# Kernel tuning notes

Hardware: AMD Instinct MI355X
Metric: run time of the kernel (lower is better)

Reference implementation:

```python
import jax, jax.numpy as jnp
import numpy as np

B, T, C, H = 2, 2048, 2048, 16
D = C // H  # head size = 128
ROPE_BASE = 10000.0


def setup_inputs() -> dict:
    key = jax.random.key(0)
    k1, k2, k3 = jax.random.split(key, 3)
    scale = 1.0 / np.sqrt(C)
    x = jax.random.normal(k1, (B, T, C), dtype=jnp.float32)
    w_qkv = jax.random.normal(k2, (3 * C, C), dtype=jnp.float32) * scale
    w_o = jax.random.normal(k3, (C, C), dtype=jnp.float32) * scale
    # rope cache: complex exp(i * pos * theta_j), stored as cos/sin, shape [T, D//2]
    inv_freq = 1.0 / (ROPE_BASE ** (np.arange(0, D, 2, dtype=np.float32) / D))  # [D//2]
    angles = np.arange(T, dtype=np.float32)[:, None] * inv_freq[None, :]        # [T, D//2]
    rope_cos = jnp.asarray(np.cos(angles))
    rope_sin = jnp.asarray(np.sin(angles))
    return {"x": x, "w_qkv": w_qkv, "w_o": w_o, "rope_cos": rope_cos, "rope_sin": rope_sin}


def _apply_rope(x, cos, sin):
    # x: [B, T, H, D]; cos/sin: [T, D//2]
    xr = x.reshape(*x.shape[:-1], D // 2, 2)
    x0, x1 = xr[..., 0], xr[..., 1]
    c = cos[None, :, None, :]
    s = sin[None, :, None, :]
    # complex multiply (x0 + i x1) * (c + i s)
    out = jnp.stack([x0 * c - x1 * s, x0 * s + x1 * c], axis=-1)
    return out.reshape(x.shape)


def reference(x, w_qkv, w_o, rope_cos, rope_sin):
    Bs, Ts, Cs = x.shape
    qkv = jnp.einsum('btc,ec->bte', x, w_qkv)  # [B, T, 3C]
    q, k, v = jnp.split(qkv, 3, axis=-1)
    q = q.reshape(Bs, Ts, H, D)
    k = k.reshape(Bs, Ts, H, D)
    v = v.reshape(Bs, Ts, H, D)
    q = _apply_rope(q, rope_cos[:Ts], rope_sin[:Ts])
    k = _apply_rope(k, rope_cos[:Ts], rope_sin[:Ts])
    scores = jnp.einsum('bthd,bshd->bhts', q, k) / jnp.sqrt(jnp.float32(D))
    causal = jnp.tril(jnp.ones((Ts, Ts), dtype=bool))
    scores = jnp.where(causal[None, None], scores, jnp.finfo(scores.dtype).min)
    attn = jax.nn.softmax(scores, axis=-1)
    y = jnp.einsum('bhts,bshd->bthd', attn, v).reshape(Bs, Ts, Cs)
    return jnp.einsum('btc,oc->bto', y, w_o)
```

## Files before the change

### kernel.cpp

```cpp
#include <hip/hip_runtime.h>
#include <cstdint>
#include <cstddef>

#define DEVI __device__ __forceinline__

typedef __attribute__((ext_vector_type(8))) short short8;
typedef __attribute__((ext_vector_type(4))) float f32x4;
typedef __attribute__((ext_vector_type(16))) float f32x16;
typedef __attribute__((ext_vector_type(4))) unsigned int u32x4;

static constexpr int Bdim = 2, T = 2048, C = 2048, H = 16, D = 128;
static constexpr int CQ = 3 * C;

DEVI unsigned short f2bf(float f) {
  unsigned int u = __float_as_uint(f);
  u = (u + 0x7fffu + ((u >> 16) & 1u)) >> 16;
  return (unsigned short)u;
}
DEVI float bf2f(unsigned int u) { return __uint_as_float(u << 16); }

DEVI unsigned int cvtpk(float lo, float hi) {
  unsigned int r;
  asm("v_cvt_pk_bf16_f32 %0, %1, %2" : "=v"(r) : "v"(lo), "v"(hi));
  return r;
}

DEVI void gload_lds16(const void* g, void* l) {
  __builtin_amdgcn_global_load_lds((const __attribute__((address_space(1))) void*)g,
                                   (__attribute__((address_space(3))) void*)l, 16, 0, 0);
}

__global__ __launch_bounds__(256) void convert_all(const float* __restrict__ x,
                                                   const float* __restrict__ wqkv,
                                                   const float* __restrict__ wo,
                                                   unsigned short* __restrict__ xb,
                                                   unsigned short* __restrict__ wqkvb,
                                                   unsigned short* __restrict__ wob) {
  int bid = blockIdx.x;
  const float* src;
  unsigned short* dst;
  if (bid < 8192) {
    src = x; dst = xb;
  } else if (bid < 8192 + 12288) {
    bid -= 8192; src = wqkv; dst = wqkvb;
  } else {
    bid -= 8192 + 12288; src = wo; dst = wob;
  }
  const int i = (bid * 256 + threadIdx.x) * 4;
  float4 v = *(const float4*)&src[i];
  uint2 o;
  o.x = (unsigned)f2bf(v.x) | ((unsigned)f2bf(v.y) << 16);
  o.y = (unsigned)f2bf(v.z) | ((unsigned)f2bf(v.w) << 16);
  *(uint2*)&dst[i] = o;
}

template <int OUT_BF16>
__global__ __launch_bounds__(256) void gemm_bt(const unsigned short* __restrict__ A,
                                               const unsigned short* __restrict__ Bm,
                                               void* __restrict__ outp,
                                               int M, int N, int Kd) {
  __shared__ __align__(16) unsigned short lds_a[128 * 64];
  __shared__ __align__(16) unsigned short lds_b[128 * 64];
  const int tid = threadIdx.x;
  const int wid = tid >> 6, lane = tid & 63;
  const int lg = lane >> 4, lc = lane & 15;
  const int m0 = blockIdx.y * 128, n0 = blockIdx.x * 128;
  const int wr = (wid >> 1) * 64, wc = (wid & 1) * 64;
  const int srow = wid * 8 + (lane >> 3);
  const int schunk = lane & 7;

  f32x4 acc[4][4] = {};

  for (int k0 = 0; k0 < Kd; k0 += 64) {
    __syncthreads();
#pragma unroll
    for (int j = 0; j < 4; ++j) {
      const int row = j * 32 + srow;
      const int cc = schunk ^ (row & 7);
      gload_lds16(&A[(size_t)(m0 + row) * Kd + k0 + cc * 8], &lds_a[j * 2048 + wid * 512]);
      gload_lds16(&Bm[(size_t)(n0 + row) * Kd + k0 + cc * 8], &lds_b[j * 2048 + wid * 512]);
    }
    __syncthreads();
    __builtin_amdgcn_s_setprio(1);
#pragma unroll
    for (int kk = 0; kk < 2; ++kk) {
      short8 af[4], bf[4];
#pragma unroll
      for (int m = 0; m < 4; ++m) {
        const int row = wr + m * 16 + lc;
        af[m] = *(const short8*)&lds_a[row * 64 + (((kk * 4 + lg) ^ (row & 7)) * 8)];
      }
#pragma unroll
      for (int n = 0; n < 4; ++n) {
        const int row = wc + n * 16 + lc;
        bf[n] = *(const short8*)&lds_b[row * 64 + (((kk * 4 + lg) ^ (row & 7)) * 8)];
      }
#pragma unroll
      for (int m = 0; m < 4; ++m)
#pragma unroll
        for (int n = 0; n < 4; ++n)
          acc[m][n] = __builtin_amdgcn_mfma_f32_16x16x32_bf16(af[m], bf[n], acc[m][n], 0, 0, 0);
    }
    __builtin_amdgcn_s_setprio(0);
  }

#pragma unroll
  for (int m = 0; m < 4; ++m)
#pragma unroll
    for (int n = 0; n < 4; ++n)
#pragma unroll
      for (int r = 0; r < 4; ++r) {
        const int row = m0 + wr + m * 16 + lg * 4 + r;
        const int col = n0 + wc + n * 16 + lc;
        const float v = acc[m][n][r];
        if (OUT_BF16)
          ((unsigned short*)outp)[(size_t)row * N + col] = f2bf(v);
        else
          ((float*)outp)[(size_t)row * N + col] = v;
      }
}

__global__ __launch_bounds__(256) void rope_vt_kernel(const unsigned short* __restrict__ qkv,
                                                      const float* __restrict__ cosb,
                                                      const float* __restrict__ sinb,
                                                      unsigned short* __restrict__ Qr,
                                                      unsigned short* __restrict__ Kr,
                                                      unsigned short* __restrict__ Vt) {
  if (blockIdx.x < 16384) {
    const int idx = blockIdx.x * 256 + threadIdx.x;
    const int i = idx & 63;
    const int h = (idx >> 6) & (H - 1);
    const int tg = idx >> 10;
    const int t = tg & (T - 1);
    const int b = tg >> 11;
    const float c = cosb[t * 64 + i], s = sinb[t * 64 + i];
    const unsigned short* row = qkv + (size_t)tg * CQ;
    const unsigned int q = *(const unsigned int*)&row[h * D + 2 * i];
    const unsigned int k = *(const unsigned int*)&row[C + h * D + 2 * i];
    const float q0 = bf2f(q & 0xffffu), q1 = bf2f(q >> 16);
    const float k0 = bf2f(k & 0xffffu), k1 = bf2f(k >> 16);
    const float SC = 0.08838834764831845f * 1.4426950408889634f;
    const float q0r = (q0 * c - q1 * s) * SC, q1r = (q0 * s + q1 * c) * SC;
    const float k0r = k0 * c - k1 * s, k1r = k0 * s + k1 * c;
    const size_t off = ((size_t)(b * H + h) * T + t) * D + 2 * i;
    *(unsigned int*)&Qr[off] = (unsigned)f2bf(q0r) | ((unsigned)f2bf(q1r) << 16);
    *(unsigned int*)&Kr[off] = (unsigned)f2bf(k0r) | ((unsigned)f2bf(k1r) << 16);
  } else {
    __shared__ unsigned short tile[64][65];
    const int bid2 = blockIdx.x - 16384;
    const int t0 = (bid2 & 31) * 64;
    const int d0 = ((bid2 >> 5) & 1) * 64;
    const int bh = bid2 >> 6, b = bh >> 4, h = bh & (H - 1);
    const int tx = threadIdx.x & 63, ty = threadIdx.x >> 6;
#pragma unroll
    for (int rr = 0; rr < 64; rr += 4)
      tile[rr + ty][tx] = qkv[(size_t)(b * T + t0 + rr + ty) * CQ + 2 * C + h * D + d0 + tx];
    __syncthreads();
#pragma unroll
    for (int rr = 0; rr < 64; rr += 4)
      Vt[((size_t)bh * D + d0 + rr + ty) * T + t0 + tx] = tile[tx][rr + ty];
  }
}

__global__ __launch_bounds__(256, 2) void flash_attn(const unsigned short* __restrict__ Q,
                                                     const unsigned short* __restrict__ K,
                                                     const unsigned short* __restrict__ Vt,
                                                     unsigned short* __restrict__ Y) {
  __shared__ __align__(16) unsigned short ldsK[64 * 128];
  __shared__ __align__(16) unsigned short ldsV[64 * 128];

  const int bid = blockIdx.x;
  const int lid = (bid & 7) * 64 + (bid >> 3);
  const int bh = lid >> 4;
  const int qt = 15 - (lid & 15);
  const int wid = threadIdx.x >> 6;
  const int lane = threadIdx.x & 63;
  const int l31 = lane & 31, l15 = lane & 15;
  const int hi = lane >> 5;
  const int b = bh >> 4, h = bh & (H - 1);
  const int q0w = qt * 128 + wid * 32;
  const int qrow = q0w + l31;

  const unsigned short* Qh = Q + (size_t)bh * T * D;
  const unsigned short* Kh = K + (size_t)bh * T * D;
  const unsigned short* Vh = Vt + (size_t)bh * D * T;

  const int sr = lane >> 4;

  short8 qf[8];
#pragma unroll
  for (int ds = 0; ds < 8; ++ds)
    qf[ds] = *(const short8*)&Qh[(size_t)qrow * D + ds * 16 + hi * 8];

  f32x16 oacc[4] = {};
  float m_run = -1e30f, l_run = 0.f;

  u32x4 rK[4], rV[4];

#pragma unroll
  for (int j = 0; j < 4; ++j) {
    const int r0 = (wid * 4 + j) * 4;
    const int row = r0 + sr;
    const int cc = l15 ^ (row & 15);
    rK[j] = *(const u32x4*)&Kh[(size_t)row * D + cc * 8];
    const int cv = l15 ^ (row & 15);
    const int d = row + ((cv >> 3) << 6);
    rV[j] = *(const u32x4*)&Vh[(size_t)d * T + (cv & 7) * 8];
  }

  const int ntb = 2 * qt + 2;
  for (int t = 0; t < ntb; ++t) {
    const int kv0 = t * 64;

    __builtin_amdgcn_s_barrier();

#pragma unroll
    for (int j = 0; j < 4; ++j) {
      const int r0 = (wid * 4 + j) * 4;
      *(u32x4*)((char*)ldsK + r0 * 256 + lane * 16) = rK[j];
      *(u32x4*)((char*)ldsV + r0 * 256 + lane * 16) = rV[j];
    }
    asm volatile("s_waitcnt lgkmcnt(0)" ::: "memory");
    __builtin_amdgcn_s_barrier();
    __builtin_amdgcn_sched_barrier(0);

    if (t + 1 < ntb) {
      const int kvn = kv0 + 64;
#pragma unroll
      for (int j = 0; j < 4; ++j) {
        const int r0 = (wid * 4 + j) * 4;
        const int row = r0 + sr;
        const int cc = l15 ^ (row & 15);
        rK[j] = *(const u32x4*)&Kh[(size_t)(kvn + row) * D + cc * 8];
        const int d = row + ((cc >> 3) << 6);
        rV[j] = *(const u32x4*)&Vh[(size_t)d * T + kvn + (cc & 7) * 8];
      }
    }
    __builtin_amdgcn_sched_barrier(0);

    if (kv0 <= q0w + 31) {
      f32x16 s0 = {}, s1 = {};
      __builtin_amdgcn_s_setprio(1);
#pragma unroll
      for (int ds = 0; ds < 8; ++ds) {
        const int cs = ((ds * 2 + hi) ^ l15) * 8;
        const short8 k0 = *(const short8*)&ldsK[l31 * 128 + cs];
        const short8 k1 = *(const short8*)&ldsK[(32 + l31) * 128 + cs];
        s0 = __builtin_amdgcn_mfma_f32_32x32x16_bf16(k0, qf[ds], s0, 0, 0, 0);
        s1 = __builtin_amdgcn_mfma_f32_32x32x16_bf16(k1, qf[ds], s1, 0, 0, 0);
      }
      __builtin_amdgcn_s_setprio(0);

      if (kv0 + 63 > q0w) {
#pragma unroll
        for (int r = 0; r < 16; ++r) {
          const int kvr = kv0 + (r & 3) + 8 * (r >> 2) + 4 * hi;
          s0[r] = (kvr <= qrow) ? s0[r] : -1e30f;
          s1[r] = (kvr + 32 <= qrow) ? s1[r] : -1e30f;
        }
      }

      float mt[8];
#pragma unroll
      for (int r = 0; r < 8; ++r)
        mt[r] = fmaxf(fmaxf(s0[r], s0[r + 8]), fmaxf(s1[r], s1[r + 8]));
#pragma unroll
      for (int r = 0; r < 4; ++r) mt[r] = fmaxf(mt[r], mt[r + 4]);
      float mx = fmaxf(fmaxf(mt[0], mt[1]), fmaxf(mt[2], mt[3]));
      mx = fmaxf(mx, __shfl_xor(mx, 32));
      const float mnew = fmaxf(m_run, mx);
      if (__any(mnew > m_run)) {
        const float f = exp2f(m_run - mnew);
        m_run = mnew;
        l_run *= f;
#pragma unroll
        for (int blk = 0; blk < 4; ++blk) oacc[blk] *= f;
      }
#pragma unroll
      for (int r = 0; r < 16; ++r) {
        s0[r] = exp2f(s0[r] - m_run);
        s1[r] = exp2f(s1[r] - m_run);
      }
      {
        float a0 = 0.f, a1 = 0.f, a2 = 0.f, a3 = 0.f;
#pragma unroll
        for (int r = 0; r < 16; r += 4) {
          a0 += s0[r] + s1[r];
          a1 += s0[r + 1] + s1[r + 1];
          a2 += s0[r + 2] + s1[r + 2];
          a3 += s0[r + 3] + s1[r + 3];
        }
        l_run += (a0 + a1) + (a2 + a3);
      }

      __builtin_amdgcn_s_setprio(1);
#pragma unroll
      for (int ks = 0; ks < 4; ++ks) {
        const int rb = (ks & 1) * 8;
        const f32x16& S = (ks < 2) ? s0 : s1;
        const unsigned int w0 = cvtpk(S[rb + 0], S[rb + 1]);
        const unsigned int w1 = cvtpk(S[rb + 2], S[rb + 3]);
        const unsigned int w2 = cvtpk(S[rb + 4], S[rb + 5]);
        const unsigned int w3 = cvtpk(S[rb + 6], S[rb + 7]);
        const unsigned int x0 = (unsigned int)__shfl_xor((int)w0, 32);
        const unsigned int x1 = (unsigned int)__shfl_xor((int)w1, 32);
        const unsigned int x2 = (unsigned int)__shfl_xor((int)w2, 32);
        const unsigned int x3 = (unsigned int)__shfl_xor((int)w3, 32);
        u32x4 av;
        av[0] = hi ? x2 : w0;
        av[1] = hi ? x3 : w1;
        av[2] = hi ? w2 : x0;
        av[3] = hi ? w3 : x1;
        const short8 pf = __builtin_bit_cast(short8, av);
#pragma unroll
        for (int blk = 0; blk < 4; ++blk) {
          const int row2 = (blk & 1) * 32 + l31;
          const int cs = ((((blk >> 1) * 8) + ks * 2 + hi) ^ l15) * 8;
          const short8 vf = *(const short8*)&ldsV[row2 * 128 + cs];
          oacc[blk] = __builtin_amdgcn_mfma_f32_32x32x16_bf16(vf, pf, oacc[blk], 0, 0, 0);
        }
      }
      __builtin_amdgcn_s_setprio(0);
    }
  }

  const float l = l_run + __shfl_xor(l_run, 32);
  const float inv = 1.0f / l;
  unsigned short* yrow = Y + ((size_t)(b * T + qrow)) * C + h * D;
#pragma unroll
  for (int blk = 0; blk < 4; ++blk)
#pragma unroll
    for (int g = 0; g < 4; ++g) {
      const int d0 = blk * 32 + 8 * g + 4 * hi;
      uint2 st;
      st.x = cvtpk(oacc[blk][4 * g + 0] * inv, oacc[blk][4 * g + 1] * inv);
      st.y = cvtpk(oacc[blk][4 * g + 2] * inv, oacc[blk][4 * g + 3] * inv);
      *(uint2*)&yrow[d0] = st;
    }
}

extern "C" void kernel_launch(void* const* d_in, const int* in_sizes, int n_in,
                              void* d_out, int out_size, void* d_ws, size_t ws_size,
                              hipStream_t stream) {
  const float* x = (const float*)d_in[0];
  const float* wqkv = (const float*)d_in[1];
  const float* wo = (const float*)d_in[2];
  const float* rc = (const float*)d_in[3];
  const float* rs = (const float*)d_in[4];
  float* out = (float*)d_out;
  char* ws = (char*)d_ws;

  unsigned short* xb    = (unsigned short*)(ws + 0);
  unsigned short* wqkvb = (unsigned short*)(ws + 16777216);
  unsigned short* qkv   = (unsigned short*)(ws + 41943040);
  unsigned short* Qr    = (unsigned short*)(ws + 92274688);
  unsigned short* Kr    = (unsigned short*)(ws + 109051904);
  unsigned short* wob   = (unsigned short*)(ws + 125829120);
  unsigned short* Vt  = xb;
  unsigned short* Yb  = qkv;

  convert_all<<<8192 + 12288 + 4096, 256, 0, stream>>>(x, wqkv, wo, xb, wqkvb, wob);
  gemm_bt<1><<<dim3(CQ / 128, (Bdim * T) / 128), 256, 0, stream>>>(xb, wqkvb, (void*)qkv,
                                                                   Bdim * T, CQ, C);
  rope_vt_kernel<<<18432, 256, 0, stream>>>(qkv, rc, rs, Qr, Kr, Vt);
  flash_attn<<<512, 256, 0, stream>>>(Qr, Kr, Vt, Yb);
  gemm_bt<0><<<dim3(C / 128, (Bdim * T) / 128), 256, 0, stream>>>(Yb, wob, (void*)out,
                                                                  Bdim * T, C, C);
}
```

Baseline: 267.2 us.

## Fuse RoPE into flash attention and keep only V transpose pre-pass

Removes the separate RoPE kernel that wrote rotated Q and K buffers. The attention kernel now reads Q and K directly from the qkv projection output and applies the rotation in registers while loading, with the K rotation done before the LDS store. A standalone V transpose kernel remains. This saves a full write and read of Q/K, but it adds cos/sin loads and rotation ALU work for every K tile visit, which raises register pressure and redundant compute.

New measurement: 306.1 us. 1.15x slower.

```diff
diff --git a/kernel.cpp b/kernel.cpp
--- a/kernel.cpp
+++ b/kernel.cpp
@@ -120,51 +120,25 @@
       }
 }
 
-__global__ __launch_bounds__(256) void rope_vt_kernel(const unsigned short* __restrict__ qkv,
-                                                      const float* __restrict__ cosb,
-                                                      const float* __restrict__ sinb,
-                                                      unsigned short* __restrict__ Qr,
-                                                      unsigned short* __restrict__ Kr,
-                                                      unsigned short* __restrict__ Vt) {
-  if (blockIdx.x < 16384) {
-    const int idx = blockIdx.x * 256 + threadIdx.x;
-    const int i = idx & 63;
-    const int h = (idx >> 6) & (H - 1);
-    const int tg = idx >> 10;
-    const int t = tg & (T - 1);
-    const int b = tg >> 11;
-    const float c = cosb[t * 64 + i], s = sinb[t * 64 + i];
-    const unsigned short* row = qkv + (size_t)tg * CQ;
-    const unsigned int q = *(const unsigned int*)&row[h * D + 2 * i];
-    const unsigned int k = *(const unsigned int*)&row[C + h * D + 2 * i];
-    const float q0 = bf2f(q & 0xffffu), q1 = bf2f(q >> 16);
-    const float k0 = bf2f(k & 0xffffu), k1 = bf2f(k >> 16);
-    const float SC = 0.08838834764831845f * 1.4426950408889634f;
-    const float q0r = (q0 * c - q1 * s) * SC, q1r = (q0 * s + q1 * c) * SC;
-    const float k0r = k0 * c - k1 * s, k1r = k0 * s + k1 * c;
-    const size_t off = ((size_t)(b * H + h) * T + t) * D + 2 * i;
-    *(unsigned int*)&Qr[off] = (unsigned)f2bf(q0r) | ((unsigned)f2bf(q1r) << 16);
-    *(unsigned int*)&Kr[off] = (unsigned)f2bf(k0r) | ((unsigned)f2bf(k1r) << 16);
-  } else {
-    __shared__ unsigned short tile[64][65];
-    const int bid2 = blockIdx.x - 16384;
-    const int t0 = (bid2 & 31) * 64;
-    const int d0 = ((bid2 >> 5) & 1) * 64;
-    const int bh = bid2 >> 6, b = bh >> 4, h = bh & (H - 1);
-    const int tx = threadIdx.x & 63, ty = threadIdx.x >> 6;
-#pragma unroll
-    for (int rr = 0; rr < 64; rr += 4)
-      tile[rr + ty][tx] = qkv[(size_t)(b * T + t0 + rr + ty) * CQ + 2 * C + h * D + d0 + tx];
-    __syncthreads();
-#pragma unroll
-    for (int rr = 0; rr < 64; rr += 4)
-      Vt[((size_t)bh * D + d0 + rr + ty) * T + t0 + tx] = tile[tx][rr + ty];
-  }
-}
-
-__global__ __launch_bounds__(256, 2) void flash_attn(const unsigned short* __restrict__ Q,
-                                                     const unsigned short* __restrict__ K,
+__global__ __launch_bounds__(256) void transpose_v(const unsigned short* __restrict__ qkv,
+                                                   unsigned short* __restrict__ Vt) {
+  __shared__ unsigned short tile[64][65];
+  const int bh = blockIdx.z, b = bh >> 4, h = bh & (H - 1);
+  const int t0 = blockIdx.x * 64, d0 = blockIdx.y * 64;
+  const int tx = threadIdx.x & 63, ty = threadIdx.x >> 6;
+#pragma unroll
+  for (int rr = 0; rr < 64; rr += 4)
+    tile[rr + ty][tx] = qkv[(size_t)(b * T + t0 + rr + ty) * CQ + 2 * C + h * D + d0 + tx];
+  __syncthreads();
+#pragma unroll
+  for (int rr = 0; rr < 64; rr += 4)
+    Vt[((size_t)bh * D + d0 + rr + ty) * T + t0 + tx] = tile[tx][rr + ty];
+}
+
+__global__ __launch_bounds__(256, 2) void flash_attn(const unsigned short* __restrict__ qkv,
                                                      const unsigned short* __restrict__ Vt,
+                                                     const float* __restrict__ cosb,
+                                                     const float* __restrict__ sinb,
                                                      unsigned short* __restrict__ Y) {
   __shared__ __align__(16) unsigned short ldsK[64 * 128];
   __shared__ __align__(16) unsigned short ldsV[64 * 128];
@@ -181,31 +155,45 @@
   const int q0w = qt * 128 + wid * 32;
   const int qrow = q0w + l31;
 
-  const unsigned short* Qh = Q + (size_t)bh * T * D;
-  const unsigned short* Kh = K + (size_t)bh * T * D;
+  const unsigned short* Qq = qkv + (size_t)(b * T) * CQ + h * D;
+  const unsigned short* Kq = qkv + (size_t)(b * T) * CQ + C + h * D;
   const unsigned short* Vh = Vt + (size_t)bh * D * T;
 
   const int sr = lane >> 4;
 
+  const float SC = 0.08838834764831845f * 1.4426950408889634f;
   short8 qf[8];
 #pragma unroll
-  for (int ds = 0; ds < 8; ++ds)
-    qf[ds] = *(const short8*)&Qh[(size_t)qrow * D + ds * 16 + hi * 8];
+  for (int ds = 0; ds < 8; ++ds) {
+    const int d0 = ds * 16 + hi * 8;
+    const u32x4 raw = *(const u32x4*)&Qq[(size_t)qrow * CQ + d0];
+    const f32x4 c4 = *(const f32x4*)&cosb[qrow * 64 + (d0 >> 1)];
+    const f32x4 s4 = *(const f32x4*)&sinb[qrow * 64 + (d0 >> 1)];
+    u32x4 w;
+#pragma unroll
+    for (int e = 0; e < 4; ++e) {
+      const float x0 = bf2f(raw[e] & 0xffffu), x1 = bf2f(raw[e] >> 16);
+      w[e] = cvtpk((x0 * c4[e] - x1 * s4[e]) * SC, (x0 * s4[e] + x1 * c4[e]) * SC);
+    }
+    qf[ds] = __builtin_bit_cast(short8, w);
+  }
 
   f32x16 oacc[4] = {};
   float m_run = -1e30f, l_run = 0.f;
 
   u32x4 rK[4], rV[4];
+  f32x4 rC[4], rS[4];
 
 #pragma unroll
   for (int j = 0; j < 4; ++j) {
     const int r0 = (wid * 4 + j) * 4;
     const int row = r0 + sr;
     const int cc = l15 ^ (row & 15);
-    rK[j] = *(const u32x4*)&Kh[(size_t)row * D + cc * 8];
-    const int cv = l15 ^ (row & 15);
-    const int d = row + ((cv >> 3) << 6);
-    rV[j] = *(const u32x4*)&Vh[(size_t)d * T + (cv & 7) * 8];
+    rK[j] = *(const u32x4*)&Kq[(size_t)row * CQ + cc * 8];
+    rC[j] = *(const f32x4*)&cosb[row * 64 + cc * 4];
+    rS[j] = *(const f32x4*)&sinb[row * 64 + cc * 4];
+    const int d = row + ((cc >> 3) << 6);
+    rV[j] = *(const u32x4*)&Vh[(size_t)d * T + (cc & 7) * 8];
   }
 
   const int ntb = 2 * qt + 2;
@@ -217,7 +205,13 @@
 #pragma unroll
     for (int j = 0; j < 4; ++j) {
       const int r0 = (wid * 4 + j) * 4;
-      *(u32x4*)((char*)ldsK + r0 * 256 + lane * 16) = rK[j];
+      u32x4 w;
+#pragma unroll
+      for (int e = 0; e < 4; ++e) {
+        const float x0 = bf2f(rK[j][e] & 0xffffu), x1 = bf2f(rK[j][e] >> 16);
+        w[e] = cvtpk(x0 * rC[j][e] - x1 * rS[j][e], x0 * rS[j][e] + x1 * rC[j][e]);
+      }
+      *(u32x4*)((char*)ldsK + r0 * 256 + lane * 16) = w;
       *(u32x4*)((char*)ldsV + r0 * 256 + lane * 16) = rV[j];
     }
     asm volatile("s_waitcnt lgkmcnt(0)" ::: "memory");
@@ -231,7 +225,9 @@
         const int r0 = (wid * 4 + j) * 4;
         const int row = r0 + sr;
         const int cc = l15 ^ (row & 15);
-        rK[j] = *(const u32x4*)&Kh[(size_t)(kvn + row) * D + cc * 8];
+        rK[j] = *(const u32x4*)&Kq[(size_t)(kvn + row) * CQ + cc * 8];
+        rC[j] = *(const f32x4*)&cosb[(kvn + row) * 64 + cc * 4];
+        rS[j] = *(const f32x4*)&sinb[(kvn + row) * 64 + cc * 4];
         const int d = row + ((cc >> 3) << 6);
         rV[j] = *(const u32x4*)&Vh[(size_t)d * T + kvn + (cc & 7) * 8];
       }
@@ -353,17 +349,15 @@
   unsigned short* xb    = (unsigned short*)(ws + 0);
   unsigned short* wqkvb = (unsigned short*)(ws + 16777216);
   unsigned short* qkv   = (unsigned short*)(ws + 41943040);
-  unsigned short* Qr    = (unsigned short*)(ws + 92274688);
-  unsigned short* Kr    = (unsigned short*)(ws + 109051904);
+  unsigned short* Yb    = (unsigned short*)(ws + 92274688);
+  unsigned short* Vt    = (unsigned short*)(ws + 109051904);
   unsigned short* wob   = (unsigned short*)(ws + 125829120);
-  unsigned short* Vt  = xb;
-  unsigned short* Yb  = qkv;
 
   convert_all<<<8192 + 12288 + 4096, 256, 0, stream>>>(x, wqkv, wo, xb, wqkvb, wob);
   gemm_bt<1><<<dim3(CQ / 128, (Bdim * T) / 128), 256, 0, stream>>>(xb, wqkvb, (void*)qkv,
                                                                    Bdim * T, CQ, C);
-  rope_vt_kernel<<<18432, 256, 0, stream>>>(qkv, rc, rs, Qr, Kr, Vt);
-  flash_attn<<<512, 256, 0, stream>>>(Qr, Kr, Vt, Yb);
+  transpose_v<<<dim3(T / 64, D / 64, Bdim * H), 256, 0, stream>>>(qkv, Vt);
+  flash_attn<<<512, 256, 0, stream>>>(qkv, Vt, rc, rs, Yb);
   gemm_bt<0><<<dim3(C / 128, (Bdim * T) / 128), 256, 0, stream>>>(Yb, wob, (void*)out,
                                                                   Bdim * T, C, C);
 }
```

## Split causal attention KV range into two halves and merge with a combine kernel

Applied to the files above, without the earlier changes.

Each query tile's causal KV loop is split into two halves, run by separate blocks, so the flash-attention grid doubles from 512 to 1024 blocks. The aim is to cut the critical path of the longest causal tiles and improve load balance across CUs. Each half writes a bf16 partial output plus per-row (max, sum) statistics. A new combine kernel rescales and merges the two partials before the output projection. The cost is an extra launch, extra global traffic for two partial outputs and the stats, and an extra bf16 rounding of the partials.

Result: no change. 262.0 us (median of 3 runs) (-1.9%).

```diff
diff --git a/kernel.cpp b/kernel.cpp
--- a/kernel.cpp
+++ b/kernel.cpp
@@ -165,14 +165,17 @@
 __global__ __launch_bounds__(256, 2) void flash_attn(const unsigned short* __restrict__ Q,
                                                      const unsigned short* __restrict__ K,
                                                      const unsigned short* __restrict__ Vt,
-                                                     unsigned short* __restrict__ Y) {
+                                                     unsigned short* __restrict__ OA,
+                                                     unsigned short* __restrict__ OB,
+                                                     float2* __restrict__ ml) {
   __shared__ __align__(16) unsigned short ldsK[64 * 128];
   __shared__ __align__(16) unsigned short ldsV[64 * 128];
 
   const int bid = blockIdx.x;
-  const int lid = (bid & 7) * 64 + (bid >> 3);
-  const int bh = lid >> 4;
-  const int qt = 15 - (lid & 15);
+  const int lid = (bid & 7) * 128 + (bid >> 3);
+  const int bh = lid >> 5;
+  const int qt = 15 - ((lid >> 1) & 15);
+  const int hf = lid & 1;
   const int wid = threadIdx.x >> 6;
   const int lane = threadIdx.x & 63;
   const int l31 = lane & 31, l15 = lane & 15;
@@ -186,6 +189,8 @@
   const unsigned short* Vh = Vt + (size_t)bh * D * T;
 
   const int sr = lane >> 4;
+  const int tstart = hf ? (qt + 1) : 0;
+  const int tend = hf ? (2 * qt + 2) : (qt + 1);
 
   short8 qf[8];
 #pragma unroll
@@ -202,14 +207,12 @@
     const int r0 = (wid * 4 + j) * 4;
     const int row = r0 + sr;
     const int cc = l15 ^ (row & 15);
-    rK[j] = *(const u32x4*)&Kh[(size_t)row * D + cc * 8];
-    const int cv = l15 ^ (row & 15);
-    const int d = row + ((cv >> 3) << 6);
-    rV[j] = *(const u32x4*)&Vh[(size_t)d * T + (cv & 7) * 8];
-  }
-
-  const int ntb = 2 * qt + 2;
-  for (int t = 0; t < ntb; ++t) {
+    rK[j] = *(const u32x4*)&Kh[(size_t)(tstart * 64 + row) * D + cc * 8];
+    const int d = row + ((cc >> 3) << 6);
+    rV[j] = *(const u32x4*)&Vh[(size_t)d * T + tstart * 64 + (cc & 7) * 8];
+  }
+
+  for (int t = tstart; t < tend; ++t) {
     const int kv0 = t * 64;
 
     __builtin_amdgcn_s_barrier();
@@ -224,7 +227,7 @@
     __builtin_amdgcn_s_barrier();
     __builtin_amdgcn_sched_barrier(0);
 
-    if (t + 1 < ntb) {
+    if (t + 1 < tend) {
       const int kvn = kv0 + 64;
 #pragma unroll
       for (int j = 0; j < 4; ++j) {
@@ -325,8 +328,8 @@
   }
 
   const float l = l_run + __shfl_xor(l_run, 32);
-  const float inv = 1.0f / l;
-  unsigned short* yrow = Y + ((size_t)(b * T + qrow)) * C + h * D;
+  const float inv = (l > 0.f) ? (1.0f / l) : 0.f;
+  unsigned short* yrow = (hf ? OB : OA) + ((size_t)(b * T + qrow)) * C + h * D;
 #pragma unroll
   for (int blk = 0; blk < 4; ++blk)
 #pragma unroll
@@ -337,6 +340,41 @@
       st.y = cvtpk(oacc[blk][4 * g + 2] * inv, oacc[blk][4 * g + 3] * inv);
       *(uint2*)&yrow[d0] = st;
     }
+  if (hi == 0) {
+    float2 v;
+    v.x = m_run;
+    v.y = l;
+    ml[(size_t)hf * (Bdim * H * T) + (size_t)bh * T + qrow] = v;
+  }
+}
+
+__global__ __launch_bounds__(256) void combine_halves(const unsigned short* __restrict__ OA,
+                                                      const unsigned short* __restrict__ OB,
+                                                      const float2* __restrict__ ml,
+                                                      unsigned short* __restrict__ Y) {
+  const int i = blockIdx.x * 256 + threadIdx.x;
+  const int d0 = (i & 15) * 8;
+  const int rowid = i >> 4;
+  const int bh = rowid >> 11, t = rowid & (T - 1);
+  const int b = bh >> 4, h = bh & (H - 1);
+  const float2 a = ml[rowid];
+  const float2 bb = ml[(size_t)(Bdim * H * T) + rowid];
+  const float m = fmaxf(a.x, bb.x);
+  const float wA = a.y * exp2f(a.x - m);
+  const float wB = bb.y * exp2f(bb.x - m);
+  const float den = wA + wB;
+  const float fA = wA / den, fB = wB / den;
+  const size_t off = ((size_t)(b * T + t)) * C + h * D + d0;
+  const u32x4 ra = *(const u32x4*)&OA[off];
+  const u32x4 rb = *(const u32x4*)&OB[off];
+  u32x4 w;
+#pragma unroll
+  for (int e = 0; e < 4; ++e) {
+    const float o0 = bf2f(ra[e] & 0xffffu) * fA + bf2f(rb[e] & 0xffffu) * fB;
+    const float o1 = bf2f(ra[e] >> 16) * fA + bf2f(rb[e] >> 16) * fB;
+    w[e] = cvtpk(o0, o1);
+  }
+  *(u32x4*)&Y[off] = w;
 }
 
 extern "C" void kernel_launch(void* const* d_in, const int* in_sizes, int n_in,
@@ -357,13 +395,17 @@
   unsigned short* Kr    = (unsigned short*)(ws + 109051904);
   unsigned short* wob   = (unsigned short*)(ws + 125829120);
   unsigned short* Vt  = xb;
-  unsigned short* Yb  = qkv;
+  unsigned short* OA  = (unsigned short*)(ws + 41943040);
+  unsigned short* OB  = (unsigned short*)(ws + 58720256);
+  float2*         ml  = (float2*)(ws + 75497472);
+  unsigned short* Yf  = Qr;
 
   convert_all<<<8192 + 12288 + 4096, 256, 0, stream>>>(x, wqkv, wo, xb, wqkvb, wob);
   gemm_bt<1><<<dim3(CQ / 128, (Bdim * T) / 128), 256, 0, stream>>>(xb, wqkvb, (void*)qkv,
                                                                    Bdim * T, CQ, C);
   rope_vt_kernel<<<18432, 256, 0, stream>>>(qkv, rc, rs, Qr, Kr, Vt);
-  flash_attn<<<512, 256, 0, stream>>>(Qr, Kr, Vt, Yb);
-  gemm_bt<0><<<dim3(C / 128, (Bdim * T) / 128), 256, 0, stream>>>(Yb, wob, (void*)out,
+  flash_attn<<<1024, 256, 0, stream>>>(Qr, Kr, Vt, OA, OB, ml);
+  combine_halves<<<4096, 256, 0, stream>>>(OA, OB, ml, Yf);
+  gemm_bt<0><<<dim3(C / 128, (Bdim * T) / 128), 256, 0, stream>>>(Yf, wob, (void*)out,
                                                                   Bdim * T, C, C);
 }
```
